# Kernel tuning notes

Hardware: AMD Instinct MI355X
Metric: run time of the kernel (lower is better)

Reference implementation:

```python
import jax, jax.numpy as jnp
import numpy as np
import jax.scipy.linalg as jsp

H = 8
C = 64
D_CONV = 4
EPS_L2 = 1e-6
EPS_RMS = 1e-5


def l2norm(x):
    return x * jax.lax.rsqrt(jnp.sum(x * x, axis=-1, keepdims=True) + EPS_L2)


def setup_inputs() -> dict:
    key = jax.random.key(0)
    ks = jax.random.split(key, 12)
    B, T, D = 4, 4096, 1024
    x = jax.random.normal(ks[0], (B, T, D), dtype=jnp.float32)
    s = 0.02
    Wv = jax.random.normal(ks[1], (D, D), dtype=jnp.float32) * s
    Wg = jax.random.normal(ks[2], (D, D), dtype=jnp.float32) * s
    Wo = jax.random.normal(ks[3], (D, D), dtype=jnp.float32) * s
    Wb = jax.random.normal(ks[4], (H, D), dtype=jnp.float32) * s
    Wa = jax.random.normal(ks[5], (H, D), dtype=jnp.float32) * s
    # dt_bias / A_log initialized as in the torch module
    u = jax.random.uniform(ks[6], (H,))
    dt = jnp.exp(u * (jnp.log(0.1) - jnp.log(0.001)) + jnp.log(0.001))
    dt_bias = dt + jnp.log(-jnp.expm1(-dt))
    A_log = jnp.log(jax.random.uniform(ks[7], (H,)) * 16.0 + 1e-4)
    norm_w = jnp.ones((D // H,), dtype=jnp.float32)
    conv_w = jax.random.normal(ks[8], (D, D_CONV), dtype=jnp.float32) * 0.1
    conv_b = jnp.zeros((D,), dtype=jnp.float32)
    return {"x": x, "Wv": Wv, "Wg": Wg, "Wo": Wo, "Wb": Wb, "Wa": Wa,
            "dt_bias": dt_bias, "A_log": A_log, "norm_w": norm_w,
            "conv_w": conv_w, "conv_b": conv_b}


def _causal_depthwise_conv(x, w, b):
    # x: (B,T,D), w: (D,d_conv) -- causal depthwise conv1d
    B, T, D = x.shape
    xp = jnp.pad(x, ((0, 0), (D_CONV - 1, 0), (0, 0)))
    out = b
    for j in range(D_CONV):
        out = out + xp[:, j:j + T] * w[:, j]
    return out


def _forward(x, Wv, Wg, Wo, Wb, Wa, dt_bias, A_log, norm_w, conv_w, conv_b):
    B, T, D = x.shape
    K = D // H
    n = T // C  # T chosen as a multiple of C, so pad_len == 0

    rk = l2norm(x.reshape(B, T, H, K)) / np.sqrt(K)
    x_shift = jnp.pad(x[:, :-1], ((0, 0), (1, 0), (0, 0)))
    wk = l2norm(x_shift.reshape(B, T, H, K))
    v = jax.nn.silu(_causal_depthwise_conv(x @ Wv.T, conv_w, conv_b)).reshape(B, T, H, K)
    gate = (x @ Wg.T).reshape(B, T, H, K)
    beta = jax.nn.sigmoid(x @ Wb.T)                       # (B,T,H)
    decay = -jnp.exp(A_log) * jax.nn.softplus(x @ Wa.T + dt_bias)  # (B,T,H)

    # -> (B,H,T,K)
    rk, wk, v = (jnp.transpose(t, (0, 2, 1, 3)) for t in (rk, wk, v))
    beta_t = jnp.transpose(beta, (0, 2, 1))[..., None]    # (B,H,T,1)
    v = v * beta_t
    wk_beta = wk * beta_t

    # chunk: (B,H,n,C,K)
    ch = lambda t: t.reshape(B, H, n, C, K)
    rk, wk, v, wk_beta = ch(rk), ch(wk), ch(v), ch(wk_beta)
    decay = jnp.cumsum(jnp.transpose(decay, (0, 2, 1)).reshape(B, H, n, C), axis=-1)
    decay_exp = jnp.exp(decay)[..., None]                 # (B,H,n,C,1)

    tril = jnp.tril(jnp.ones((C, C), dtype=bool))
    strict_lower = jnp.tril(jnp.ones((C, C), dtype=bool), k=-1)
    diff = decay[..., :, None] - decay[..., None, :]
    L_mask = jnp.where(tril, jnp.exp(jnp.where(tril, diff, 0.0)), 0.0)  # (B,H,n,C,C)

    A_strict = jnp.where(strict_lower,
                         -(jnp.einsum('bhnck,bhndk->bhncd', wk_beta, wk) * L_mask), 0.0)
    # forward-substitution loop == inverse of unit-lower-triangular (I - A_strict)
    eye = jnp.eye(C, dtype=x.dtype)
    Tmat = jsp.solve_triangular(eye - A_strict,
                                jnp.broadcast_to(eye, A_strict.shape),
                                lower=True)
    v = Tmat @ v
    wk_cumdecay = Tmat @ (wk_beta * decay_exp)

    # scan over chunks maintaining state S: (B,H,K,K)
    def step(S, inp):
        rk_i, wk_i, v_i, wkc_i, L_i, dec_i = inp
        attn = jnp.where(tril, jnp.einsum('bhck,bhdk->bhcd', rk_i, wk_i) * L_i, 0.0)
        v_new = v_i - wkc_i @ S
        o_inter = (rk_i * jnp.exp(dec_i)[..., None]) @ S
        o_i = o_inter + attn @ v_new
        dw = jnp.exp(dec_i[..., -1:] - dec_i)[..., None]
        S_new = S * jnp.exp(dec_i[..., -1])[..., None, None] + \
            jnp.einsum('bhck,bhcv->bhkv', wk_i * dw, v_new)
        return S_new, o_i

    mv = lambda t: jnp.moveaxis(t, 2, 0)  # chunk axis to front
    S0 = jnp.zeros((B, H, K, K), dtype=x.dtype)
    _, o = jax.lax.scan(step, S0, (mv(rk), mv(wk), mv(v), mv(wk_cumdecay),
                                   mv(L_mask), mv(decay)))
    # o: (n,B,H,C,K) -> (B,T,H,K)
    o = jnp.transpose(o, (1, 0, 3, 2, 4)).reshape(B, T, H, K)

    # per-head RMSNorm, gated, output projection
    o = o * jax.lax.rsqrt(jnp.mean(o * o, axis=-1, keepdims=True) + EPS_RMS) * norm_w
    o = o * jax.nn.silu(gate)
    return o.reshape(B, T, D) @ Wo.T


def reference(x, Wv, Wg, Wo, Wb, Wa, dt_bias, A_log, norm_w, conv_w, conv_b):
    return _forward(x, Wv, Wg, Wo, Wb, Wa, dt_bias, A_log, norm_w, conv_w, conv_b)
```

## Files before the change

### kernel.cpp

```cpp
#include <hip/hip_runtime.h>
#include <hip/hip_bf16.h>
#include <math.h>

#define H_ 8
#define K_ 128
#define C_ 64
#define D_ 1024
#define T_ 4096
#define B_ 4
#define N_CH 64
#define BT_ (B_*T_)

typedef __attribute__((ext_vector_type(8))) short bf16x8;
typedef __attribute__((ext_vector_type(4))) float f32x4;
typedef __hip_bfloat16 bf16;

__device__ __forceinline__ float siluf(float x){ return x / (1.0f + expf(-x)); }
__device__ __forceinline__ float expn(float x){ return expf(fminf(x, 0.f)); }
__device__ __forceinline__ float sanf(float v){ return (__builtin_fabsf(v) <= 1e30f) ? v : 0.f; }

__device__ __forceinline__ void ld_bf8(const bf16* p, float* o){
  uint4 u = *(const uint4*)p;
  o[0]=__uint_as_float(u.x<<16); o[1]=__uint_as_float(u.x&0xffff0000u);
  o[2]=__uint_as_float(u.y<<16); o[3]=__uint_as_float(u.y&0xffff0000u);
  o[4]=__uint_as_float(u.z<<16); o[5]=__uint_as_float(u.z&0xffff0000u);
  o[6]=__uint_as_float(u.w<<16); o[7]=__uint_as_float(u.w&0xffff0000u);
}
__device__ __forceinline__ void ld_bf8s(const bf16* p, float* o){
  ld_bf8(p, o);
#pragma unroll
  for (int e=0;e<8;e++) o[e] = sanf(o[e]);
}
__device__ __forceinline__ void ld_bf4(const bf16* p, float* o){
  uint2 u = *(const uint2*)p;
  o[0]=__uint_as_float(u.x<<16); o[1]=__uint_as_float(u.x&0xffff0000u);
  o[2]=__uint_as_float(u.y<<16); o[3]=__uint_as_float(u.y&0xffff0000u);
}
__device__ __forceinline__ void ld_bf4s(const bf16* p, float* o){
  ld_bf4(p, o);
#pragma unroll
  for (int e=0;e<4;e++) o[e] = sanf(o[e]);
}
__device__ __forceinline__ unsigned short f2bfu(float f){
  bf16 h = __float2bfloat16(f);
  return *reinterpret_cast<unsigned short*>(&h);
}
__device__ __forceinline__ uint2 pack_bf4(const float* v){
  uint2 r;
  r.x = (unsigned)f2bfu(v[0]) | ((unsigned)f2bfu(v[1])<<16);
  r.y = (unsigned)f2bfu(v[2]) | ((unsigned)f2bfu(v[3])<<16);
  return r;
}

__global__ __launch_bounds__(256) void cast_f2b(
    const float* __restrict__ src, bf16* __restrict__ dst, int n4)
{
  int i = blockIdx.x*256 + threadIdx.x;
  if (i >= n4) return;
  float4 v = *(const float4*)&src[(size_t)i*4];
  float a[4] = {v.x, v.y, v.z, v.w};
  *(uint2*)&dst[(size_t)i*4] = pack_bf4(a);
}

template<typename OUT_T>
__global__ __launch_bounds__(256) void gemm_bt_mfma(
    const bf16* __restrict__ X, const bf16* __restrict__ W,
    OUT_T* __restrict__ Y, int M, int N, int K)
{
  __shared__ __align__(16) bf16 As[128][72];
  __shared__ __align__(16) bf16 Bs[128][72];
  const int tid = threadIdx.x;
  const int wv = tid >> 6;
  const int lane = tid & 63;
  const int row0 = blockIdx.y*128, col0 = blockIdx.x*128;
  const int mw = (wv&1)*64, nw = (wv>>1)*64;
  const int q = lane >> 4;
  const int l15 = lane & 15;
  f32x4 acc[4][4];
#pragma unroll
  for (int mi=0;mi<4;mi++)
#pragma unroll
    for (int ni=0;ni<4;ni++) acc[mi][ni] = (f32x4){0.f,0.f,0.f,0.f};

  const int lr = tid >> 3;
  const int lc = (tid & 7) * 8;
  for (int k0=0;k0<K;k0+=64){
#pragma unroll
    for (int i=0;i<4;i++){
      int r = lr + i*32;
      *(uint4*)&As[r][lc] = *(const uint4*)&X[(size_t)(row0+r)*K + k0 + lc];
      *(uint4*)&Bs[r][lc] = *(const uint4*)&W[(size_t)(col0+r)*K + k0 + lc];
    }
    __syncthreads();
#pragma unroll
    for (int ks=0; ks<64; ks+=32){
      bf16x8 af[4], bfr[4];
#pragma unroll
      for (int i=0;i<4;i++){
        af[i]  = *(const bf16x8*)&As[mw + i*16 + l15][ks + q*8];
        bfr[i] = *(const bf16x8*)&Bs[nw + i*16 + l15][ks + q*8];
      }
#pragma unroll
      for (int mi=0;mi<4;mi++)
#pragma unroll
        for (int ni=0;ni<4;ni++)
          acc[mi][ni] = __builtin_amdgcn_mfma_f32_16x16x32_bf16(af[mi], bfr[ni], acc[mi][ni], 0,0,0);
    }
    __syncthreads();
  }
#pragma unroll
  for (int mi=0;mi<4;mi++){
#pragma unroll
    for (int reg=0;reg<4;reg++){
      int row = row0 + mw + mi*16 + q*4 + reg;
#pragma unroll
      for (int ni=0;ni<4;ni++){
        int col = col0 + nw + ni*16 + l15;
        if constexpr (sizeof(OUT_T) == 2)
          Y[(size_t)row*N + col] = (OUT_T)__float2bfloat16(acc[mi][ni][reg]);
        else
          Y[(size_t)row*N + col] = (OUT_T)acc[mi][ni][reg];
      }
    }
  }
}

__global__ __launch_bounds__(256) void proj_small(
    const float* __restrict__ x, const float* __restrict__ Wb, const float* __restrict__ Wa,
    const float* __restrict__ dt_bias, const float* __restrict__ A_log,
    float* __restrict__ beta_out, float* __restrict__ dec_out)
{
  const int w = threadIdx.x >> 6;
  const int lane = threadIdx.x & 63;
  const int bt = blockIdx.x*4 + w;
  const int b = bt >> 12, t = bt & (T_-1);
  const float* xr = x + (size_t)bt*D_;
  float xv[16];
#pragma unroll
  for (int p=0;p<4;p++){
    float4 v = *(const float4*)&xr[lane*16 + p*4];
    xv[p*4+0]=v.x; xv[p*4+1]=v.y; xv[p*4+2]=v.z; xv[p*4+3]=v.w;
  }
  float accb[H_], acca[H_];
#pragma unroll
  for (int h=0;h<H_;h++){
    float sb=0.f, sa=0.f;
#pragma unroll
    for (int p=0;p<4;p++){
      float4 wb = *(const float4*)&Wb[(size_t)h*D_ + lane*16 + p*4];
      float4 wa = *(const float4*)&Wa[(size_t)h*D_ + lane*16 + p*4];
      sb += xv[p*4+0]*wb.x + xv[p*4+1]*wb.y + xv[p*4+2]*wb.z + xv[p*4+3]*wb.w;
      sa += xv[p*4+0]*wa.x + xv[p*4+1]*wa.y + xv[p*4+2]*wa.z + xv[p*4+3]*wa.w;
    }
    accb[h]=sb; acca[h]=sa;
  }
#pragma unroll
  for (int h=0;h<H_;h++){
#pragma unroll
    for (int m=1;m<64;m<<=1){
      accb[h] += __shfl_xor(accb[h], m, 64);
      acca[h] += __shfl_xor(acca[h], m, 64);
    }
  }
  if (lane < H_) {
    int h = lane;
    beta_out[(size_t)(b*H_+h)*T_ + t] = 1.f/(1.f+expf(-accb[h]));
  } else if (lane < 2*H_) {
    int h = lane - H_;
    float z = acca[h] + dt_bias[h];
    float sp = fmaxf(z,0.f) + log1pf(expf(-fabsf(z)));
    dec_out[(size_t)(b*H_+h)*T_ + t] = -expf(A_log[h]) * sp;
  }
}

__global__ __launch_bounds__(256) void xinv_kernel(
    const float* __restrict__ x, float* __restrict__ xinv)
{
  const int bt = blockIdx.x;
  const int b = bt >> 12, t = bt & (T_-1);
  const int tid = threadIdx.x;
  float4 xv = *(const float4*)&x[(size_t)bt*D_ + tid*4];
  float ss = xv.x*xv.x + xv.y*xv.y + xv.z*xv.z + xv.w*xv.w;
#pragma unroll
  for (int m=1;m<32;m<<=1) ss += __shfl_xor(ss, m, 32);
  const int h = tid >> 5;
  if ((tid & 31) == 0)
    xinv[(size_t)(b*H_+h)*T_ + t] = rsqrtf(ss + 1e-6f);
}

__global__ __launch_bounds__(256) void cumsum_dec(
    const float* __restrict__ dec_raw, float* __restrict__ dec_cum)
{
  int g = blockIdx.x*4 + (threadIdx.x>>6);
  int lane = threadIdx.x & 63;
  float v = sanf(dec_raw[(size_t)g*C_ + lane]);
#pragma unroll
  for (int off=1; off<64; off<<=1){
    float u = __shfl_up(v, off, 64);
    if (lane >= off) v += u;
  }
  dec_cum[(size_t)g*C_ + lane] = v;
}

__global__ __launch_bounds__(256) void chunk_prep(
    const bf16* __restrict__ xb, const float* __restrict__ xinv,
    const bf16* __restrict__ vpre, const float* __restrict__ cw, const float* __restrict__ cb,
    const float* __restrict__ beta, const float* __restrict__ dec,
    bf16* __restrict__ vchk, bf16* __restrict__ wkc, bf16* __restrict__ attn)
{
  __shared__ __align__(16) bf16 s_x[65][136];
  __shared__ __align__(16) float s_a[64][64];
  __shared__ float s_dec[64], s_beta[64], s_invsh[64], s_negbi[64], s_rsc[64], s_sc2[64];

  const int tid = threadIdx.x;
  const int chunk = blockIdx.x;
  const int bh = chunk >> 6;
  const int nc = chunk & 63;
  const int b = bh >> 3, h = bh & 7;
  const int t0 = nc * C_;
  const size_t xrow = (size_t)b*T_;
  const size_t rowb = (size_t)bh*T_ + t0;
  const size_t kobase = rowb * K_;
  const int w = tid >> 6;
  const int lane = tid & 63;
  const int l15 = lane & 15;
  const int q = lane >> 4;

  for (int idx = tid; idx < 65*16; idx += 256){
    int r = idx >> 4;
    int seg = (idx & 15) * 8;
    int t = t0 + r - 1;
    int tr = t < 0 ? 0 : t;
    *(uint4*)&s_x[r][seg] = *(const uint4*)&xb[(xrow + tr)*D_ + h*K_ + seg];
  }
  if (tid < C_){
    int c = tid;
    float dv  = sanf(dec[rowb + c]);
    float bet = sanf(beta[rowb + c]);
    float invc = sanf(xinv[rowb + c]);
    int tm1 = t0 + c - 1;
    float ivs = (tm1 >= 0) ? sanf(xinv[(size_t)bh*T_ + tm1]) : 0.f;
    s_dec[c] = dv;
    s_beta[c] = bet;
    s_invsh[c] = ivs;
    s_negbi[c] = -bet * ivs;
    s_rsc[c] = invc * 0.08838834764831845f;
    s_sc2[c] = ivs * bet * expn(dv);
  }
  __syncthreads();

  bf16x8 aG[4], aT[4];
#pragma unroll
  for (int ks=0; ks<4; ks++){
    aG[ks] = *(const bf16x8*)&s_x[16*w + l15][ks*32 + q*8];
    aT[ks] = *(const bf16x8*)&s_x[16*w + l15 + 1][ks*32 + q*8];
  }
  f32x4 accG[4], accT[4];
#pragma unroll
  for (int J=0;J<4;J++){ accG[J]=(f32x4){0.f,0.f,0.f,0.f}; accT[J]=(f32x4){0.f,0.f,0.f,0.f}; }
#pragma unroll
  for (int J=0;J<4;J++){
    if (J <= w){
#pragma unroll
      for (int ks=0; ks<4; ks++){
        bf16x8 bfrag = *(const bf16x8*)&s_x[16*J + l15][ks*32 + q*8];
        accG[J] = __builtin_amdgcn_mfma_f32_16x16x32_bf16(aG[ks], bfrag, accG[J], 0,0,0);
        accT[J] = __builtin_amdgcn_mfma_f32_16x16x32_bf16(aT[ks], bfrag, accT[J], 0,0,0);
      }
    }
  }
  {
    const int i0 = 16*w + q*4;
#pragma unroll
    for (int J=0;J<4;J++){
      const int j = 16*J + l15;
#pragma unroll
      for (int reg=0;reg<4;reg++){
        const int i = i0 + reg;
        if (j < i)
          s_a[i][j] = s_negbi[i] * s_invsh[j] * expn(s_dec[i]-s_dec[j]) * accG[J][reg];
        float val = 0.f;
        if (j <= i)
          val = s_rsc[i] * s_invsh[j] * expn(s_dec[i]-s_dec[j]) * accT[J][reg];
        attn[(size_t)chunk*4096 + i*64 + j] = __float2bfloat16(val);
      }
    }
  }

  float v[64];
  if (tid < 128){
    const int col = tid;
    float4 cwv = *(const float4*)&cw[(h*K_+col)*4];
    const float cbv = cb[h*K_+col];
    const bf16* vp = vpre + (xrow + t0)*D_ + h*K_ + col;
    float win0, win1, win2;
    { int t = t0-3; win0 = (t>=0)? sanf(__bfloat162float(vpre[(xrow+t)*D_+h*K_+col])) : 0.f; }
    { int t = t0-2; win1 = (t>=0)? sanf(__bfloat162float(vpre[(xrow+t)*D_+h*K_+col])) : 0.f; }
    { int t = t0-1; win2 = (t>=0)? sanf(__bfloat162float(vpre[(xrow+t)*D_+h*K_+col])) : 0.f; }
#pragma unroll
    for (int c8=0; c8<8; c8++){
      float nv[8];
#pragma unroll
      for (int u=0;u<8;u++) nv[u] = sanf(__bfloat162float(vp[(size_t)(c8*8+u)*D_]));
#pragma unroll
      for (int u=0;u<8;u++){
        const int c = c8*8+u;
        float a = cbv + cwv.x*win0 + cwv.y*win1 + cwv.z*win2 + cwv.w*nv[u];
        v[c] = siluf(a) * s_beta[c];
        win0=win1; win1=win2; win2=nv[u];
      }
    }
  } else {
    const int col = tid - 128;
#pragma unroll
    for (int c=0;c<64;c++)
      v[c] = __bfloat162float(s_x[c][col]) * s_sc2[c];
  }
  __syncthreads();

#pragma unroll
  for (int i=1;i<64;i++){
    const float* ar = s_a[i];
    float s0=0.f, s1=0.f, s2=0.f, s3=0.f;
    int j=0;
#pragma unroll
    for (; j+4<=i; j+=4){
      float4 a4 = *(const float4*)&ar[j];
      s0 += a4.x*v[j+0]; s1 += a4.y*v[j+1];
      s2 += a4.z*v[j+2]; s3 += a4.w*v[j+3];
    }
#pragma unroll
    for (; j<i; j++) s0 += ar[j]*v[j];
    v[i] += (s0+s2)+(s1+s3);
  }

  {
    const int col = tid & 127;
    bf16* dst = (tid < 128 ? vchk : wkc) + kobase + col;
#pragma unroll
    for (int c=0;c<64;c++)
      dst[(size_t)c*K_] = __float2bfloat16(v[c]);
  }
}

__global__ __launch_bounds__(256) void scan_kernel(
    const bf16* __restrict__ xb, const float* __restrict__ xinv,
    bf16* vo, const bf16* __restrict__ wkc,
    const bf16* __restrict__ attn, const float* __restrict__ dec)
{
  __shared__ __align__(16) bf16 a_wkc[C_][136];
  __shared__ __align__(16) bf16 a_x  [C_][136];
  __shared__ __align__(16) bf16 xst  [K_][72];
  __shared__ __align__(16) bf16 a_att[C_][72];
  __shared__ __align__(16) bf16 st_hi[16][136];
  __shared__ __align__(16) bf16 st_lo[16][136];
  __shared__ __align__(16) bf16 vn_t [16][72];
  __shared__ __align__(16) bf16 vn_sh[16][72];
  __shared__ __align__(16) bf16 vn_sl[16][72];
  __shared__ __align__(16) float s_o[C_];
  __shared__ __align__(16) float s_scv[C_];
  __shared__ float s_a63;

  const int tid = threadIdx.x;
  const int bh = blockIdx.x & 31;
  const int g  = blockIdx.x >> 5;
  const int b = bh >> 3, h = bh & 7;
  const int j0 = g*16;
  const int w  = tid >> 6;
  const int lane = tid & 63;
  const int l15 = lane & 15;
  const int q = lane >> 4;
  const int wrow = 16*w;
  const size_t xrow = (size_t)b*T_;

  {
    unsigned short* z1 = (unsigned short*)&st_hi[0][0];
    unsigned short* z2 = (unsigned short*)&st_lo[0][0];
    for (int e=tid; e<16*136; e+=256){ z1[e]=0; z2[e]=0; }
  }
  f32x4 accS[2];
#pragma unroll
  for (int s2=0;s2<2;s2++) accS[s2] = (f32x4){0.f,0.f,0.f,0.f};

  const int r_st = tid >> 2;
  const int k8   = (tid & 3) * 8;

  for (int nc=0; nc<N_CH; nc++){
    const int t0 = nc*C_;
    const size_t rowb = (size_t)bh*T_ + t0;

    if (tid < C_){
      float dv  = sanf(dec[rowb + tid]);
      float d63 = sanf(dec[rowb + 63]);
      s_o[tid] = sanf(xinv[(size_t)bh*T_ + t0 + tid]) * 0.08838834764831845f * expn(dv);
      int tm1 = t0 + tid - 1;
      float invp = (tm1 >= 0) ? sanf(xinv[(size_t)bh*T_ + tm1]) : 0.f;
      s_scv[tid] = invp * expn(d63 - dv);
      if (tid == 63) s_a63 = expn(d63);
    }
    {
      const bf16* pw = wkc + (rowb + r_st)*K_ + k8;
      const bf16* px = xb + (xrow + t0 + r_st)*D_ + h*K_ + k8;
#pragma unroll
      for (int i=0;i<4;i++){
        uint4 u = *(const uint4*)(pw + i*32);
        u.x ^= 0x80008000u; u.y ^= 0x80008000u; u.z ^= 0x80008000u; u.w ^= 0x80008000u;
        *(uint4*)&a_wkc[r_st][k8 + i*32] = u;
        *(uint4*)&a_x[r_st][k8 + i*32] = *(const uint4*)(px + i*32);
      }
    }
    {
      const bf16* pa = attn + (size_t)(bh*N_CH + nc)*4096 + r_st*64 + k8;
      *(uint4*)&a_att[r_st][k8]      = *(const uint4*)pa;
      *(uint4*)&a_att[r_st][k8 + 32] = *(const uint4*)(pa + 32);
    }
    {
      const int c0 = (tid & 31)*2;
      const int kb2 = (tid >> 5)*16;
      int t1 = t0 + c0 - 1;
      const bf16* p1 = xb + (xrow + (t1 < 0 ? 0 : t1))*D_ + h*K_ + kb2;
      const bf16* p2 = xb + (xrow + (t0 + c0))*D_ + h*K_ + kb2;
      uint4 ua = *(const uint4*)p1, ub = *(const uint4*)(p1+8);
      uint4 uc = *(const uint4*)p2, ud = *(const uint4*)(p2+8);
      unsigned r1[8] = {ua.x,ua.y,ua.z,ua.w,ub.x,ub.y,ub.z,ub.w};
      unsigned r2[8] = {uc.x,uc.y,uc.z,uc.w,ud.x,ud.y,ud.z,ud.w};
#pragma unroll
      for (int i2=0;i2<8;i2++){
        *(unsigned*)&xst[kb2 + 2*i2][c0]     = (r1[i2] & 0xffffu) | (r2[i2] << 16);
        *(unsigned*)&xst[kb2 + 2*i2 + 1][c0] = (r1[i2] >> 16) | (r2[i2] & 0xffff0000u);
      }
    }
    float vinit[4];
    {
      const bf16* pv = vo + (rowb + wrow + q*4)*K_ + j0 + l15;
#pragma unroll
      for (int r=0;r<4;r++) vinit[r] = __bfloat162float(pv[(size_t)r*K_]);
    }
    __syncthreads();

    f32x4 accV;
#pragma unroll
    for (int r=0;r<4;r++) accV[r] = vinit[r];
    f32x4 accP = (f32x4){0.f,0.f,0.f,0.f};
#pragma unroll
    for (int ks=0; ks<4; ks++){
      bf16x8 bh_ = *(const bf16x8*)&st_hi[l15][ks*32 + q*8];
      bf16x8 bl_ = *(const bf16x8*)&st_lo[l15][ks*32 + q*8];
      bf16x8 a1 = *(const bf16x8*)&a_wkc[wrow + l15][ks*32 + q*8];
      bf16x8 a2 = *(const bf16x8*)&a_x  [wrow + l15][ks*32 + q*8];
      accV = __builtin_amdgcn_mfma_f32_16x16x32_bf16(a1, bh_, accV, 0,0,0);
      accV = __builtin_amdgcn_mfma_f32_16x16x32_bf16(a1, bl_, accV, 0,0,0);
      accP = __builtin_amdgcn_mfma_f32_16x16x32_bf16(a2, bh_, accP, 0,0,0);
      accP = __builtin_amdgcn_mfma_f32_16x16x32_bf16(a2, bl_, accP, 0,0,0);
    }
    f32x4 sov  = *(const f32x4*)&s_o[wrow + q*4];
    f32x4 scvv = *(const f32x4*)&s_scv[wrow + q*4];
    f32x4 oacc;
#pragma unroll
    for (int r=0;r<4;r++) oacc[r] = accP[r] * sov[r];
    {
      float v4[4] = {accV[0],accV[1],accV[2],accV[3]};
      *(uint2*)&vn_t[l15][wrow + q*4] = pack_bf4(v4);
      float vs[4];
#pragma unroll
      for (int r=0;r<4;r++) vs[r] = accV[r] * scvv[r];
      uint2 ph = pack_bf4(vs);
      float lo4[4];
      lo4[0] = vs[0] - __uint_as_float(ph.x << 16);
      lo4[1] = vs[1] - __uint_as_float(ph.x & 0xffff0000u);
      lo4[2] = vs[2] - __uint_as_float(ph.y << 16);
      lo4[3] = vs[3] - __uint_as_float(ph.y & 0xffff0000u);
      *(uint2*)&vn_sh[l15][wrow + q*4] = ph;
      *(uint2*)&vn_sl[l15][wrow + q*4] = pack_bf4(lo4);
    }
    __syncthreads();

#pragma unroll
    for (int ks=0; ks<2; ks++){
      bf16x8 aA = *(const bf16x8*)&a_att[wrow + l15][ks*32 + q*8];
      bf16x8 bV = *(const bf16x8*)&vn_t[l15][ks*32 + q*8];
      oacc = __builtin_amdgcn_mfma_f32_16x16x32_bf16(aA, bV, oacc, 0,0,0);
    }
    {
      bf16* po = vo + (rowb + wrow + q*4)*K_ + j0 + l15;
#pragma unroll
      for (int r=0;r<4;r++) po[(size_t)r*K_] = __float2bfloat16(oacc[r]);
    }
    {
      const float a63 = s_a63;
#pragma unroll
      for (int sub=0; sub<2; sub++){
        f32x4 acc = accS[sub];
#pragma unroll
        for (int r=0;r<4;r++) acc[r] *= a63;
#pragma unroll
        for (int ks=0; ks<2; ks++){
          bf16x8 aH = *(const bf16x8*)&vn_sh[l15][ks*32 + q*8];
          bf16x8 aL = *(const bf16x8*)&vn_sl[l15][ks*32 + q*8];
          bf16x8 bX = *(const bf16x8*)&xst[32*w + 16*sub + l15][ks*32 + q*8];
          acc = __builtin_amdgcn_mfma_f32_16x16x32_bf16(aH, bX, acc, 0,0,0);
          acc = __builtin_amdgcn_mfma_f32_16x16x32_bf16(aL, bX, acc, 0,0,0);
        }
        accS[sub] = acc;
#pragma unroll
        for (int r=0;r<4;r++){
          float sv = acc[r];
          bf16 hb = __float2bfloat16(sv);
          st_hi[q*4+r][32*w + 16*sub + l15] = hb;
          st_lo[q*4+r][32*w + 16*sub + l15] = __float2bfloat16(sv - __bfloat162float(hb));
        }
      }
    }
    __syncthreads();
  }
}

__global__ __launch_bounds__(256) void norm_gate(
    const bf16* __restrict__ o, bf16* gio, const float* __restrict__ norm_w)
{
  const int bt = blockIdx.x;
  const int b = bt >> 12, t = bt & (T_-1);
  const int tid = threadIdx.x;
  const int h = tid >> 5;
  const int kk = (tid & 31)*4;
  float ov[4];
  ld_bf4s(o + ((size_t)(b*H_+h)*T_ + t)*K_ + kk, ov);
  float ss = ov[0]*ov[0] + ov[1]*ov[1] + ov[2]*ov[2] + ov[3]*ov[3];
#pragma unroll
  for (int m=1;m<32;m<<=1) ss += __shfl_xor(ss, m, 32);
  float r = rsqrtf(ss*(1.f/128.f) + 1e-5f);
  float4 nw = *(const float4*)&norm_w[kk];
  float gv[4];
  ld_bf4s(gio + (size_t)bt*D_ + tid*4, gv);
  float res[4];
  res[0] = ov[0]*r*nw.x * siluf(gv[0]);
  res[1] = ov[1]*r*nw.y * siluf(gv[1]);
  res[2] = ov[2]*r*nw.z * siluf(gv[2]);
  res[3] = ov[3]*r*nw.w * siluf(gv[3]);
  *(uint2*)&gio[(size_t)bt*D_ + tid*4] = pack_bf4(res);
}

extern "C" void kernel_launch(void* const* d_in, const int* in_sizes, int n_in,
                              void* d_out, int out_size, void* d_ws, size_t ws_size,
                              hipStream_t stream)
{
  const float* x       = (const float*)d_in[0];
  const float* Wv      = (const float*)d_in[1];
  const float* Wg      = (const float*)d_in[2];
  const float* Wo      = (const float*)d_in[3];
  const float* Wb      = (const float*)d_in[4];
  const float* Wa      = (const float*)d_in[5];
  const float* dt_bias = (const float*)d_in[6];
  const float* A_log   = (const float*)d_in[7];
  const float* norm_w  = (const float*)d_in[8];
  const float* conv_w  = (const float*)d_in[9];
  const float* conv_b  = (const float*)d_in[10];
  float* out = (float*)d_out;

  const size_t BTD = (size_t)B_*T_*D_;
  const size_t BHT = (size_t)B_*H_*T_;
  const size_t DD  = (size_t)D_*D_;

  float* beta = (float*)d_ws;
  float* decr = beta + BHT;
  float* decc = decr + BHT;
  float* xinv = decc + BHT;
  bf16* Wvb = (bf16*)(xinv + BHT);
  bf16* Wgb = Wvb + DD;
  bf16* Wob = Wgb + DD;
  bf16* xb   = Wob + DD;
  bf16* vpre = xb + BTD;
  bf16* wkc  = vpre + BTD;
  bf16* vo   = (bf16*)d_out;
  bf16* attn = vo + BTD;

  dim3 gemm_grid(D_/128, BT_/128);
  cast_f2b<<<(BTD/4+255)/256, 256, 0, stream>>>(x, xb, BTD/4);
  cast_f2b<<<(DD/4+255)/256, 256, 0, stream>>>(Wv, Wvb, DD/4);
  cast_f2b<<<(DD/4+255)/256, 256, 0, stream>>>(Wg, Wgb, DD/4);
  cast_f2b<<<(DD/4+255)/256, 256, 0, stream>>>(Wo, Wob, DD/4);
  gemm_bt_mfma<bf16><<<gemm_grid, 256, 0, stream>>>(xb, Wvb, vpre, BT_, D_, D_);
  proj_small<<<BT_/4, 256, 0, stream>>>(x, Wb, Wa, dt_bias, A_log, beta, decr);
  xinv_kernel<<<BT_, 256, 0, stream>>>(x, xinv);
  cumsum_dec<<<(BHT/C_)/4, 256, 0, stream>>>(decr, decc);
  chunk_prep<<<B_*H_*N_CH, 256, 0, stream>>>(xb, xinv, vpre, conv_w, conv_b,
                                             beta, decc, vo , wkc, attn);
  scan_kernel<<<B_*H_*8, 256, 0, stream>>>(xb, xinv, vo, wkc, attn, decc);
  gemm_bt_mfma<bf16><<<gemm_grid, 256, 0, stream>>>(xb, Wgb, vpre, BT_, D_, D_);
  norm_gate<<<BT_, 256, 0, stream>>>(vo , vpre , norm_w);
  gemm_bt_mfma<float><<<gemm_grid, 256, 0, stream>>>(vpre, Wob, out, BT_, D_, D_);
}
```

Baseline: 672.1 us.

## Double the scan grid, prefetch next chunk in registers, fuse x cast into xinv

The scan kernel now gives each block 8 value columns instead of 16, which doubles the grid from 256 to 512 blocks so more CUs are busy. Only half the lanes store output. The next chunk's global loads are issued into registers right after the barrier, so they overlap the current chunk's MFMA work, and s_setprio raises wave priority around the MFMA sections. The x-to-bf16 cast is folded into xinv_kernel, which removes one full pass over x. In exchange, each block redoes the full 16-wide state-column matmul, so that MFMA work is doubled, and register pressure goes up.

```diff
diff --git a/kernel.cpp b/kernel.cpp
--- a/kernel.cpp
+++ b/kernel.cpp
@@ -174,12 +174,14 @@
 }
 
 __global__ __launch_bounds__(256) void xinv_kernel(
-    const float* __restrict__ x, float* __restrict__ xinv)
+    const float* __restrict__ x, float* __restrict__ xinv, bf16* __restrict__ xb)
 {
   const int bt = blockIdx.x;
   const int b = bt >> 12, t = bt & (T_-1);
   const int tid = threadIdx.x;
   float4 xv = *(const float4*)&x[(size_t)bt*D_ + tid*4];
+  float a[4] = {xv.x, xv.y, xv.z, xv.w};
+  *(uint2*)&xb[(size_t)bt*D_ + tid*4] = pack_bf4(a);
   float ss = xv.x*xv.x + xv.y*xv.y + xv.z*xv.z + xv.w*xv.w;
 #pragma unroll
   for (int m=1;m<32;m<<=1) ss += __shfl_xor(ss, m, 32);
@@ -365,7 +367,7 @@
   const int bh = blockIdx.x & 31;
   const int g  = blockIdx.x >> 5;
   const int b = bh >> 3, h = bh & 7;
-  const int j0 = g*16;
+  const int j0 = g*8;
   const int w  = tid >> 6;
   const int lane = tid & 63;
   const int l15 = lane & 15;
@@ -384,64 +386,89 @@
 
   const int r_st = tid >> 2;
   const int k8   = (tid & 3) * 8;
-
-  for (int nc=0; nc<N_CH; nc++){
+  const int c0   = (lane & 31)*2 + (tid & 64);
+  (void)c0;
+  const int xc0 = (tid & 31)*2;
+  const int xkb = (tid >> 5)*16;
+
+  uint4 pf_w[4], pf_x[4], pf_a[2], pf_t[4];
+  bf16 pf_v[4];
+  float pf_d = 0.f, pf_d63 = 0.f, pf_i = 0.f, pf_ip = 0.f;
+
+  auto issue = [&](int nc){
     const int t0 = nc*C_;
     const size_t rowb = (size_t)bh*T_ + t0;
-
+    const bf16* pw = wkc + (rowb + r_st)*K_ + k8;
+    const bf16* px = xb + (xrow + t0 + r_st)*D_ + h*K_ + k8;
+#pragma unroll
+    for (int i=0;i<4;i++){
+      pf_w[i] = *(const uint4*)(pw + i*32);
+      pf_x[i] = *(const uint4*)(px + i*32);
+    }
+    const bf16* pa = attn + (size_t)(bh*N_CH + nc)*4096 + r_st*64 + k8;
+    pf_a[0] = *(const uint4*)pa;
+    pf_a[1] = *(const uint4*)(pa + 32);
+    int t1 = t0 + xc0 - 1;
+    const bf16* p1 = xb + (xrow + (t1 < 0 ? 0 : t1))*D_ + h*K_ + xkb;
+    const bf16* p2 = xb + (xrow + (t0 + xc0))*D_ + h*K_ + xkb;
+    pf_t[0] = *(const uint4*)p1; pf_t[1] = *(const uint4*)(p1+8);
+    pf_t[2] = *(const uint4*)p2; pf_t[3] = *(const uint4*)(p2+8);
+    const bf16* pv = vo + (rowb + wrow + q*4)*K_ + j0 + l15;
+#pragma unroll
+    for (int r=0;r<4;r++) pf_v[r] = pv[(size_t)r*K_];
     if (tid < C_){
-      float dv  = sanf(dec[rowb + tid]);
-      float d63 = sanf(dec[rowb + 63]);
-      s_o[tid] = sanf(xinv[(size_t)bh*T_ + t0 + tid]) * 0.08838834764831845f * expn(dv);
+      pf_d   = dec[rowb + tid];
+      pf_d63 = dec[rowb + 63];
+      pf_i   = xinv[(size_t)bh*T_ + t0 + tid];
       int tm1 = t0 + tid - 1;
-      float invp = (tm1 >= 0) ? sanf(xinv[(size_t)bh*T_ + tm1]) : 0.f;
-      s_scv[tid] = invp * expn(d63 - dv);
+      pf_ip  = (tm1 >= 0) ? xinv[(size_t)bh*T_ + tm1] : 0.f;
+    }
+  };
+
+  issue(0);
+
+  for (int nc=0; nc<N_CH; nc++){
+    const size_t rowb = (size_t)bh*T_ + (size_t)nc*C_;
+
+    if (tid < C_){
+      float dv  = sanf(pf_d);
+      float d63 = sanf(pf_d63);
+      s_o[tid] = sanf(pf_i) * 0.08838834764831845f * expn(dv);
+      s_scv[tid] = sanf(pf_ip) * expn(d63 - dv);
       if (tid == 63) s_a63 = expn(d63);
     }
+#pragma unroll
+    for (int i=0;i<4;i++){
+      uint4 u = pf_w[i];
+      u.x ^= 0x80008000u; u.y ^= 0x80008000u; u.z ^= 0x80008000u; u.w ^= 0x80008000u;
+      *(uint4*)&a_wkc[r_st][k8 + i*32] = u;
+      *(uint4*)&a_x[r_st][k8 + i*32] = pf_x[i];
+    }
+    *(uint4*)&a_att[r_st][k8]      = pf_a[0];
+    *(uint4*)&a_att[r_st][k8 + 32] = pf_a[1];
     {
-      const bf16* pw = wkc + (rowb + r_st)*K_ + k8;
-      const bf16* px = xb + (xrow + t0 + r_st)*D_ + h*K_ + k8;
-#pragma unroll
-      for (int i=0;i<4;i++){
-        uint4 u = *(const uint4*)(pw + i*32);
-        u.x ^= 0x80008000u; u.y ^= 0x80008000u; u.z ^= 0x80008000u; u.w ^= 0x80008000u;
-        *(uint4*)&a_wkc[r_st][k8 + i*32] = u;
-        *(uint4*)&a_x[r_st][k8 + i*32] = *(const uint4*)(px + i*32);
+      unsigned r1[8] = {pf_t[0].x,pf_t[0].y,pf_t[0].z,pf_t[0].w,
+                        pf_t[1].x,pf_t[1].y,pf_t[1].z,pf_t[1].w};
+      unsigned r2[8] = {pf_t[2].x,pf_t[2].y,pf_t[2].z,pf_t[2].w,
+                        pf_t[3].x,pf_t[3].y,pf_t[3].z,pf_t[3].w};
+#pragma unroll
+      for (int i2=0;i2<8;i2++){
+        *(unsigned*)&xst[xkb + 2*i2][xc0]     = (r1[i2] & 0xffffu) | (r2[i2] << 16);
+        *(unsigned*)&xst[xkb + 2*i2 + 1][xc0] = (r1[i2] >> 16) | (r2[i2] & 0xffff0000u);
       }
     }
-    {
-      const bf16* pa = attn + (size_t)(bh*N_CH + nc)*4096 + r_st*64 + k8;
-      *(uint4*)&a_att[r_st][k8]      = *(const uint4*)pa;
-      *(uint4*)&a_att[r_st][k8 + 32] = *(const uint4*)(pa + 32);
-    }
-    {
-      const int c0 = (tid & 31)*2;
-      const int kb2 = (tid >> 5)*16;
-      int t1 = t0 + c0 - 1;
-      const bf16* p1 = xb + (xrow + (t1 < 0 ? 0 : t1))*D_ + h*K_ + kb2;
-      const bf16* p2 = xb + (xrow + (t0 + c0))*D_ + h*K_ + kb2;
-      uint4 ua = *(const uint4*)p1, ub = *(const uint4*)(p1+8);
-      uint4 uc = *(const uint4*)p2, ud = *(const uint4*)(p2+8);
-      unsigned r1[8] = {ua.x,ua.y,ua.z,ua.w,ub.x,ub.y,ub.z,ub.w};
-      unsigned r2[8] = {uc.x,uc.y,uc.z,uc.w,ud.x,ud.y,ud.z,ud.w};
-#pragma unroll
-      for (int i2=0;i2<8;i2++){
-        *(unsigned*)&xst[kb2 + 2*i2][c0]     = (r1[i2] & 0xffffu) | (r2[i2] << 16);
-        *(unsigned*)&xst[kb2 + 2*i2 + 1][c0] = (r1[i2] >> 16) | (r2[i2] & 0xffff0000u);
-      }
-    }
     float vinit[4];
-    {
-      const bf16* pv = vo + (rowb + wrow + q*4)*K_ + j0 + l15;
-#pragma unroll
-      for (int r=0;r<4;r++) vinit[r] = __bfloat162float(pv[(size_t)r*K_]);
-    }
+#pragma unroll
+    for (int r=0;r<4;r++) vinit[r] = __bfloat162float(pf_v[r]);
     __syncthreads();
+
+    if (nc+1 < N_CH) issue(nc+1);
 
     f32x4 accV;
 #pragma unroll
     for (int r=0;r<4;r++) accV[r] = vinit[r];
     f32x4 accP = (f32x4){0.f,0.f,0.f,0.f};
+    __builtin_amdgcn_s_setprio(1);
 #pragma unroll
     for (int ks=0; ks<4; ks++){
       bf16x8 bh_ = *(const bf16x8*)&st_hi[l15][ks*32 + q*8];
@@ -453,6 +480,7 @@
       accP = __builtin_amdgcn_mfma_f32_16x16x32_bf16(a2, bh_, accP, 0,0,0);
       accP = __builtin_amdgcn_mfma_f32_16x16x32_bf16(a2, bl_, accP, 0,0,0);
     }
+    __builtin_amdgcn_s_setprio(0);
     f32x4 sov  = *(const f32x4*)&s_o[wrow + q*4];
     f32x4 scvv = *(const f32x4*)&s_scv[wrow + q*4];
     f32x4 oacc;
@@ -475,19 +503,22 @@
     }
     __syncthreads();
 
+    __builtin_amdgcn_s_setprio(1);
 #pragma unroll
     for (int ks=0; ks<2; ks++){
       bf16x8 aA = *(const bf16x8*)&a_att[wrow + l15][ks*32 + q*8];
       bf16x8 bV = *(const bf16x8*)&vn_t[l15][ks*32 + q*8];
       oacc = __builtin_amdgcn_mfma_f32_16x16x32_bf16(aA, bV, oacc, 0,0,0);
     }
-    {
+    __builtin_amdgcn_s_setprio(0);
+    if (l15 < 8){
       bf16* po = vo + (rowb + wrow + q*4)*K_ + j0 + l15;
 #pragma unroll
       for (int r=0;r<4;r++) po[(size_t)r*K_] = __float2bfloat16(oacc[r]);
     }
     {
       const float a63 = s_a63;
+      __builtin_amdgcn_s_setprio(1);
 #pragma unroll
       for (int sub=0; sub<2; sub++){
         f32x4 acc = accS[sub];
@@ -510,6 +541,7 @@
           st_lo[q*4+r][32*w + 16*sub + l15] = __float2bfloat16(sv - __bfloat162float(hb));
         }
       }
+      __builtin_amdgcn_s_setprio(0);
     }
     __syncthreads();
   }
@@ -575,17 +607,16 @@
   bf16* attn = vo + BTD;
 
   dim3 gemm_grid(D_/128, BT_/128);
-  cast_f2b<<<(BTD/4+255)/256, 256, 0, stream>>>(x, xb, BTD/4);
+  xinv_kernel<<<BT_, 256, 0, stream>>>(x, xinv, xb);
   cast_f2b<<<(DD/4+255)/256, 256, 0, stream>>>(Wv, Wvb, DD/4);
   cast_f2b<<<(DD/4+255)/256, 256, 0, stream>>>(Wg, Wgb, DD/4);
   cast_f2b<<<(DD/4+255)/256, 256, 0, stream>>>(Wo, Wob, DD/4);
   gemm_bt_mfma<bf16><<<gemm_grid, 256, 0, stream>>>(xb, Wvb, vpre, BT_, D_, D_);
   proj_small<<<BT_/4, 256, 0, stream>>>(x, Wb, Wa, dt_bias, A_log, beta, decr);
-  xinv_kernel<<<BT_, 256, 0, stream>>>(x, xinv);
   cumsum_dec<<<(BHT/C_)/4, 256, 0, stream>>>(decr, decc);
   chunk_prep<<<B_*H_*N_CH, 256, 0, stream>>>(xb, xinv, vpre, conv_w, conv_b,
                                              beta, decc, vo , wkc, attn);
-  scan_kernel<<<B_*H_*8, 256, 0, stream>>>(xb, xinv, vo, wkc, attn, decc);
+  scan_kernel<<<B_*H_*16, 256, 0, stream>>>(xb, xinv, vo, wkc, attn, decc);
   gemm_bt_mfma<bf16><<<gemm_grid, 256, 0, stream>>>(xb, Wgb, vpre, BT_, D_, D_);
   norm_gate<<<BT_, 256, 0, stream>>>(vo , vpre , norm_w);
   gemm_bt_mfma<float><<<gemm_grid, 256, 0, stream>>>(vpre, Wob, out, BT_, D_, D_);
```

Measured after the change: 818.4 us. 21.8% more time.
